# Kernel optimization log

Hardware: AMD Instinct MI355X
Metric: run time of the kernel (lower is better)

Reference implementation:

```python
import jax, jax.numpy as jnp
import numpy as np

B, N, G = 16, 4096, 1024
D1, D2 = 128, 256          # feature1 / feature2 channels
C_IN = D1 + D2             # 384
C_H, C_OUT = 256, 256
BN_EPS = 1e-5


def setup_inputs() -> dict:
    key = jax.random.key(0)
    ks = jax.random.split(key, 10)
    inp = {
        "feature1": jax.random.normal(ks[0], (B, D1, N), jnp.float32),
        "coord1": jax.random.normal(ks[1], (B, 3, N), jnp.float32),
        "feature2": jax.random.normal(ks[2], (B, D2, G), jnp.float32),
        "coord2": jax.random.normal(ks[3], (B, 3, G), jnp.float32),
        # conv1x1 + BN params, layer 1: 384 -> 256
        "W1": jax.random.normal(ks[4], (C_H, C_IN), jnp.float32) / np.sqrt(C_IN),
        "b1": jnp.zeros((C_H,), jnp.float32),
        "gamma1": jnp.ones((C_H,), jnp.float32),
        "beta1": jnp.zeros((C_H,), jnp.float32),
        # layer 2: 256 -> 256
        "W2": jax.random.normal(ks[5], (C_OUT, C_H), jnp.float32) / np.sqrt(C_H),
        "b2": jnp.zeros((C_OUT,), jnp.float32),
        "gamma2": jnp.ones((C_OUT,), jnp.float32),
        "beta2": jnp.zeros((C_OUT,), jnp.float32),
    }
    return inp


def _conv_bn_relu(x, W, b, gamma, beta):
    # x: [B, C_in, N]; 1x1 conv == channel GEMM
    y = jnp.einsum('oi,bin->bon', W, x) + b[None, :, None]
    m = y.mean(axis=(0, 2), keepdims=True)           # BN1d train-mode batch stats
    v = y.var(axis=(0, 2), keepdims=True)
    y = (y - m) * jax.lax.rsqrt(v + BN_EPS) * gamma[None, :, None] + beta[None, :, None]
    return jax.nn.relu(y)


def reference(feature1, coord1, feature2, coord2,
              W1, b1, gamma1, beta1, W2, b2, gamma2, beta2):
    c1 = jnp.transpose(coord1, (0, 2, 1))    # [B, N, 3]
    c2 = jnp.transpose(coord2, (0, 2, 1))    # [B, G, 3]
    f2 = jnp.transpose(feature2, (0, 2, 1))  # [B, G, D2]

    # squared pairwise distances [B, N, G]
    d = (jnp.sum(c1 * c1, -1)[:, :, None]
         + jnp.sum(c2 * c2, -1)[:, None, :]
         - 2.0 * jnp.einsum('bnd,bgd->bng', c1, c2))

    # 3 nearest neighbors (smallest distances)
    neg_d, idx = jax.lax.top_k(-d, 3)        # [B, N, 3]
    dists = -neg_d
    recip = 1.0 / (dists + 1e-8)
    weight = recip / jnp.sum(recip, axis=-1, keepdims=True)  # [B, N, 3]

    # gather neighbor features: [B, N, 3, D2]
    gathered = jnp.take_along_axis(f2[:, None, :, :], idx[:, :, :, None], axis=2)
    interp = jnp.sum(gathered * weight[..., None], axis=2)   # [B, N, D2]

    feat = jnp.concatenate([jnp.transpose(feature1, (0, 2, 1)), interp], axis=-1)
    x = jnp.transpose(feat, (0, 2, 1))       # [B, 384, N]

    x = _conv_bn_relu(x, W1, b1, gamma1, beta1)
    x = _conv_bn_relu(x, W2, b2, gamma2, beta2)
    return x
```

## Files before the change

kernel.cpp:

```cpp
#include <hip/hip_runtime.h>

#define DEVI __device__ __forceinline__

typedef unsigned short u16;
typedef unsigned int   u32;
typedef u16  u16x8 __attribute__((ext_vector_type(8)));
typedef u16  u16x4 __attribute__((ext_vector_type(4)));
typedef short bf16x8 __attribute__((ext_vector_type(8)));
typedef float f32x4 __attribute__((ext_vector_type(4)));

static constexpr int BB = 16, NN = 4096, GG = 1024;
static constexpr int D1 = 128, D2 = 256, CIN = 384, CH = 256;

DEVI float bf2f(u16 h) { u32 u = ((u32)h) << 16; float f; __builtin_memcpy(&f, &u, 4); return f; }
DEVI u16 f2bf(float f) {
    u32 u; __builtin_memcpy(&u, &f, 4);
    u32 r = (u + 0x7fffu + ((u >> 16) & 1u)) >> 16;
    return (u16)r;
}

DEVI void gload16(const void* g, void* l) {
    __builtin_amdgcn_global_load_lds((const __attribute__((address_space(1))) void*)g,
                                     (__attribute__((address_space(3))) void*)l, 16, 0, 0);
}

__global__ void k_convw(const float* __restrict__ W1, const float* __restrict__ W2,
                        u16* __restrict__ W1b, u16* __restrict__ W2b) {
    int i = blockIdx.x * 256 + threadIdx.x;
    if (i < CH * CIN) W1b[i] = f2bf(W1[i]);
    int j = i - CH * CIN;
    if (j >= 0 && j < CH * CH) W2b[j] = f2bf(W2[j]);
}

__global__ void k_f2t(const float* __restrict__ f2, u16* __restrict__ f2t) {
    int b = blockIdx.z, ct = blockIdx.y, gt = blockIdx.x;
    __shared__ u16 tile[64][65];
    int t = threadIdx.x; int g = t & 63; int q = t >> 6;
    for (int p = 0; p < 16; ++p) {
        int cl = p * 4 + q;
        tile[g][cl] = f2bf(f2[((size_t)(b * D2 + ct * 64 + cl)) * GG + gt * 64 + g]);
    }
    __syncthreads();
    for (int p = 0; p < 16; ++p) {
        int gl = p * 4 + q;
        f2t[((size_t)(b * GG + gt * 64 + gl)) * D2 + ct * 64 + g] = tile[gl][g];
    }
}

__global__ __launch_bounds__(256) void k_knn(const float* __restrict__ c1, const float* __restrict__ c2,
                                             int* __restrict__ idxo, float* __restrict__ wo) {
    int b = blockIdx.y; int t = threadIdx.x;
    int q = t >> 2, s = t & 3;
    int n = blockIdx.x * 64 + q;
    __shared__ float4 sp[GG];
    __shared__ int mi[256][4];
    const float* cb = c2 + (size_t)b * 3 * GG;
    for (int i = t; i < GG; i += 256) {
        float x = cb[i], y = cb[GG + i], z = cb[2 * GG + i];
        sp[i] = make_float4(x, y, z, x * x + y * y + z * z);
    }
    __syncthreads();
    const float* pb = c1 + (size_t)b * 3 * NN;
    float px = pb[n], py = pb[NN + n], pz = pb[2 * NN + n];
    float pn = px * px + py * py + pz * pz;
    float d0 = 3.4e38f, d1 = 3.4e38f, d2 = 3.4e38f, d3 = 3.4e38f;
    int i0 = 0, i1 = 0, i2 = 0, i3 = 0;
    for (int gb = 0; gb < GG; gb += 16) {
        #pragma unroll
        for (int u = 0; u < 4; ++u) {
            int g = gb + u * 4 + s;
            float4 p = sp[g];
            float dot = px * p.x + py * p.y + pz * p.z;
            float d = pn + p.w - 2.f * dot;
            bool c0 = d < d0, c1 = d < d1, c2 = d < d2, c3 = d < d3;
            d3 = c2 ? d2 : (c3 ? d : d3);  i3 = c2 ? i2 : (c3 ? g : i3);
            d2 = c1 ? d1 : (c2 ? d : d2);  i2 = c1 ? i1 : (c2 ? g : i2);
            d1 = c0 ? d0 : (c1 ? d : d1);  i1 = c0 ? i0 : (c1 ? g : i1);
            d0 = c0 ? d  : d0;             i0 = c0 ? g : i0;
        }
    }
    mi[t][0] = i0; mi[t][1] = i1; mi[t][2] = i2; mi[t][3] = i3;
    __syncthreads();
    if (s == 0) {
        double e0 = 1e300, e1 = 1e300, e2 = 1e300;
        int j0 = 0x7fffffff, j1 = 0x7fffffff, j2 = 0x7fffffff;
        #pragma unroll 4
        for (int k = 0; k < 16; ++k) {
            int g = mi[q * 4 + (k >> 2)][k & 3];
            float4 p = sp[g];
            double dx = (double)px - (double)p.x;
            double dy = (double)py - (double)p.y;
            double dz = (double)pz - (double)p.z;
            double d = dx * dx + dy * dy + dz * dz;
            bool lt2 = d < e2 || (d == e2 && g < j2);
            if (lt2) {
                bool lt1 = d < e1 || (d == e1 && g < j1);
                if (lt1) {
                    e2 = e1; j2 = j1;
                    bool lt0 = d < e0 || (d == e0 && g < j0);
                    if (lt0) { e1 = e0; j1 = j0; e0 = d; j0 = g; }
                    else { e1 = d; j1 = g; }
                } else { e2 = d; j2 = g; }
            }
        }
        float r0 = 1.f / ((float)e0 + 1e-8f);
        float r1 = 1.f / ((float)e1 + 1e-8f);
        float r2 = 1.f / ((float)e2 + 1e-8f);
        float sum = r0 + r1 + r2;
        size_t base = ((size_t)b * NN + n) * 3;
        idxo[base] = j0; idxo[base + 1] = j1; idxo[base + 2] = j2;
        wo[base] = r0 / sum; wo[base + 1] = r1 / sum; wo[base + 2] = r2 / sum;
    }
}

__global__ void k_pack(const float* __restrict__ f1, const u16* __restrict__ f2t,
                       const int* __restrict__ idxo, const float* __restrict__ wo,
                       u16* __restrict__ Xp) {
    int b = blockIdx.y; int n0 = blockIdx.x * 64;
    __shared__ u16 Xt[64][392];
    int t = threadIdx.x; int j = t & 63; int q = t >> 6;
    for (int p = 0; p < 4; ++p) {
        int oct = p * 4 + q; int cb = oct * 8;
        u16x8 o;
        #pragma unroll
        for (int k = 0; k < 8; ++k)
            o[k] = f2bf(f1[((size_t)(b * D1 + cb + k)) * NN + n0 + j]);
        *(u16x8*)&Xt[j][cb] = o;
    }
    size_t bn = (size_t)b * NN + n0 + j;
    int g0 = idxo[bn * 3], g1 = idxo[bn * 3 + 1], g2 = idxo[bn * 3 + 2];
    float w0 = wo[bn * 3], w1 = wo[bn * 3 + 1], w2 = wo[bn * 3 + 2];
    const u16* r0 = f2t + ((size_t)b * GG + g0) * D2;
    const u16* r1 = f2t + ((size_t)b * GG + g1) * D2;
    const u16* r2 = f2t + ((size_t)b * GG + g2) * D2;
    for (int p = 0; p < 8; ++p) {
        int oct = p * 4 + q; int cb = oct * 8;
        u16x8 a = *(const u16x8*)(r0 + cb);
        u16x8 bb = *(const u16x8*)(r1 + cb);
        u16x8 cc = *(const u16x8*)(r2 + cb);
        u16x8 o;
        #pragma unroll
        for (int k = 0; k < 8; ++k)
            o[k] = f2bf(w0 * bf2f(a[k]) + w1 * bf2f(bb[k]) + w2 * bf2f(cc[k]));
        *(u16x8*)&Xt[j][D1 + cb] = o;
    }
    __syncthreads();
    u16* dst = Xp + ((size_t)b * NN + n0) * CIN;
    for (int p = 0; p < 12; ++p) {
        int ci = p * 256 + t;
        int row = ci / 48, ch = ci % 48;
        *(u16x8*)(dst + (size_t)ci * 8) = *(const u16x8*)&Xt[row][ch * 8];
    }
}

template<int K>
__global__ __launch_bounds__(256) void k_gemm(const u16* __restrict__ A, const u16* __restrict__ Bm,
                                              const float* __restrict__ bias, u16* __restrict__ Yp,
                                              float* __restrict__ S1, float* __restrict__ S2) {
    constexpr int NK = K / 32;
    int nt = blockIdx.x, mt = blockIdx.y, b = blockIdx.z;
    int c0 = mt * 128; size_t n0 = (size_t)b * NN + nt * 128;
    __shared__ u16 Al[2][128 * 32], Bl[2][128 * 32];
    __shared__ float sred[4][64], qred[4][64];
    int t = threadIdx.x, lane = t & 63, w = t >> 6;
    int wr = w >> 1, wc = w & 1;
    f32x4 acc[4][4];
    #pragma unroll
    for (int m = 0; m < 4; ++m)
        #pragma unroll
        for (int n = 0; n < 4; ++n) acc[m][n] = (f32x4){0.f, 0.f, 0.f, 0.f};
    int lr = w * 32 + (lane >> 2);
    int lc = (lane & 3) * 8;

    #pragma unroll
    for (int i = 0; i < 2; ++i) {
        gload16(A + (size_t)(c0 + lr + i * 16) * K + lc, &Al[0][(w * 32 + i * 16) * 32]);
        gload16(Bm + (n0 + lr + i * 16) * K + lc, &Bl[0][(w * 32 + i * 16) * 32]);
    }
    __syncthreads();

    for (int ks = 0; ks < NK; ++ks) {
        int cur = ks & 1;
        if (ks + 1 < NK) {
            #pragma unroll
            for (int i = 0; i < 2; ++i) {
                gload16(A + (size_t)(c0 + lr + i * 16) * K + (ks + 1) * 32 + lc, &Al[cur ^ 1][(w * 32 + i * 16) * 32]);
                gload16(Bm + (n0 + lr + i * 16) * K + (ks + 1) * 32 + lc, &Bl[cur ^ 1][(w * 32 + i * 16) * 32]);
            }
        }
        bf16x8 af[4], bfr[4];
        #pragma unroll
        for (int m = 0; m < 4; ++m)
            af[m] = *(const bf16x8*)&Al[cur][(wr * 64 + m * 16 + (lane & 15)) * 32 + (lane >> 4) * 8];
        #pragma unroll
        for (int n = 0; n < 4; ++n)
            bfr[n] = *(const bf16x8*)&Bl[cur][(wc * 64 + n * 16 + (lane & 15)) * 32 + (lane >> 4) * 8];
        #pragma unroll
        for (int m = 0; m < 4; ++m)
            #pragma unroll
            for (int n = 0; n < 4; ++n)
                acc[m][n] = __builtin_amdgcn_mfma_f32_16x16x32_bf16(af[m], bfr[n], acc[m][n], 0, 0, 0);
        __syncthreads();
    }
    float sacc[4][4], qacc[4][4];
    #pragma unroll
    for (int m = 0; m < 4; ++m) {
        int c = c0 + wr * 64 + m * 16 + (lane >> 4) * 4;
        float b0 = bias[c], b1 = bias[c + 1], b2 = bias[c + 2], b3 = bias[c + 3];
        #pragma unroll
        for (int j = 0; j < 4; ++j) { sacc[m][j] = 0.f; qacc[m][j] = 0.f; }
        #pragma unroll
        for (int n = 0; n < 4; ++n) {
            size_t nn = n0 + wc * 64 + n * 16 + (lane & 15);
            f32x4 v = acc[m][n];
            float y0 = v[0] + b0, y1 = v[1] + b1, y2 = v[2] + b2, y3 = v[3] + b3;
            u16x4 o;
            o[0] = f2bf(y0); o[1] = f2bf(y1); o[2] = f2bf(y2); o[3] = f2bf(y3);
            *(u16x4*)(Yp + nn * CH + c) = o;
            sacc[m][0] += y0; qacc[m][0] += y0 * y0;
            sacc[m][1] += y1; qacc[m][1] += y1 * y1;
            sacc[m][2] += y2; qacc[m][2] += y2 * y2;
            sacc[m][3] += y3; qacc[m][3] += y3 * y3;
        }
    }
    #pragma unroll
    for (int m = 0; m < 4; ++m)
        #pragma unroll
        for (int j = 0; j < 4; ++j) {
            float s = sacc[m][j], qv = qacc[m][j];
            #pragma unroll
            for (int mask = 1; mask <= 8; mask <<= 1) {
                s  += __shfl_xor(s, mask);
                qv += __shfl_xor(qv, mask);
            }
            sacc[m][j] = s; qacc[m][j] = qv;
        }
    int g = lane >> 4;
    if ((lane & 15) == 0) {
        #pragma unroll
        for (int m = 0; m < 4; ++m)
            #pragma unroll
            for (int j = 0; j < 4; ++j) {
                sred[w][m * 16 + g * 4 + j] = sacc[m][j];
                qred[w][m * 16 + g * 4 + j] = qacc[m][j];
            }
    }
    __syncthreads();
    if (t < 128) {
        int half = t >> 6, cl = t & 63;
        float s  = sred[half * 2][cl] + sred[half * 2 + 1][cl];
        float qv = qred[half * 2][cl] + qred[half * 2 + 1][cl];
        atomicAdd(&S1[c0 + half * 64 + cl], s);
        atomicAdd(&S2[c0 + half * 64 + cl], qv);
    }
}

__global__ void k_fin(const float* __restrict__ S1, const float* __restrict__ S2,
                      const float* __restrict__ gamma, const float* __restrict__ beta,
                      float* __restrict__ scale, float* __restrict__ shift) {
    int c = threadIdx.x;
    float inv = 1.f / 65536.f;
    float m = S1[c] * inv;
    float v = S2[c] * inv - m * m;
    float sc = gamma[c] * rsqrtf(v + 1e-5f);
    scale[c] = sc; shift[c] = beta[c] - m * sc;
}

__global__ void k_bnrelu(const u16* __restrict__ Y, const float* __restrict__ scale,
                         const float* __restrict__ shift, u16* __restrict__ X2) {
    __shared__ float sc[256], sh[256];
    int t = threadIdx.x;
    sc[t] = scale[t]; sh[t] = shift[t];
    __syncthreads();
    size_t i = ((size_t)blockIdx.x * 256 + t) * 8;
    int c = (int)(i & 255);
    u16x8 v = *(const u16x8*)(Y + i);
    u16x8 o;
    #pragma unroll
    for (int k = 0; k < 8; ++k) {
        float f = fmaxf(sc[c + k] * bf2f(v[k]) + sh[c + k], 0.f);
        o[k] = f2bf(f);
    }
    *(u16x8*)(X2 + i) = o;
}

__global__ void k_final(const u16* __restrict__ Y2, const float* __restrict__ scale,
                        const float* __restrict__ shift, float* __restrict__ out) {
    int b = blockIdx.y, n0 = blockIdx.x * 64;
    __shared__ u16 tile[64 * 256];
    __shared__ float sc[256], sh[256];
    int t = threadIdx.x;
    sc[t] = scale[t]; sh[t] = shift[t];
    #pragma unroll
    for (int p = 0; p < 8; ++p) {
        int r = p * 8 + (t >> 5); int o = t & 31;
        u16x8 v = *(const u16x8*)(Y2 + ((size_t)(b * NN + n0 + r)) * CH + o * 8);
        int osw = o ^ (r & 7);
        *(u16x8*)&tile[r * 256 + osw * 8] = v;
    }
    __syncthreads();
    for (int p = 0; p < 64; ++p) {
        int c = p * 4 + (t >> 6); int n = t & 63;
        int osw = (c >> 3) ^ (n & 7);
        float f = bf2f(tile[n * 256 + osw * 8 + (c & 7)]);
        out[((size_t)(b * CH + c)) * NN + n0 + n] = fmaxf(sc[c] * f + sh[c], 0.f);
    }
}

extern "C" void kernel_launch(void* const* d_in, const int* in_sizes, int n_in,
                              void* d_out, int out_size, void* d_ws, size_t ws_size,
                              hipStream_t stream) {
    const float* f1  = (const float*)d_in[0];
    const float* c1  = (const float*)d_in[1];
    const float* f2  = (const float*)d_in[2];
    const float* c2  = (const float*)d_in[3];
    const float* W1  = (const float*)d_in[4];
    const float* b1  = (const float*)d_in[5];
    const float* g1  = (const float*)d_in[6];
    const float* be1 = (const float*)d_in[7];
    const float* W2  = (const float*)d_in[8];
    const float* b2  = (const float*)d_in[9];
    const float* g2  = (const float*)d_in[10];
    const float* be2 = (const float*)d_in[11];
    float* out = (float*)d_out;
    char* ws = (char*)d_ws;

    u16* Xp    = (u16*)(ws);
    u16* Y1p   = (u16*)(ws + 50331648);
    u16* X2p   = Xp;
    u16* Y2p   = Y1p;
    u16* W1b   = (u16*)(ws + 83886080);
    u16* W2b   = (u16*)(ws + 84082688);
    u16* F2t   = (u16*)(ws + 84213760);
    int*  idxo = (int*)(ws + 92602368);
    float* wo  = (float*)(ws + 93388800);
    float* stats = (float*)(ws + 94175232);
    float* S1a = stats,        *S2a = stats + 256;
    float* S1b = stats + 512,  *S2b = stats + 768;
    float* sc1 = stats + 1024, *sh1 = stats + 1280;
    float* sc2 = stats + 1536, *sh2 = stats + 1792;

    hipMemsetAsync(stats, 0, 4096, stream);
    k_convw<<<640, 256, 0, stream>>>(W1, W2, W1b, W2b);
    k_f2t<<<dim3(16, 4, 16), 256, 0, stream>>>(f2, F2t);
    k_knn<<<dim3(64, 16), 256, 0, stream>>>(c1, c2, idxo, wo);
    k_pack<<<dim3(64, 16), 256, 0, stream>>>(f1, F2t, idxo, wo, Xp);
    k_gemm<CIN><<<dim3(32, 2, 16), 256, 0, stream>>>(W1b, Xp, b1, Y1p, S1a, S2a);
    k_fin<<<1, 256, 0, stream>>>(S1a, S2a, g1, be1, sc1, sh1);
    k_bnrelu<<<8192, 256, 0, stream>>>(Y1p, sc1, sh1, X2p);
    k_gemm<CH><<<dim3(32, 2, 16), 256, 0, stream>>>(W2b, X2p, b2, Y2p, S1b, S2b);
    k_fin<<<1, 256, 0, stream>>>(S1b, S2b, g2, be2, sc2, sh2);
    k_final<<<dim3(64, 16), 256, 0, stream>>>(Y2p, sc2, sh2, out);
}
```

Baseline: 292.2 us.

## Pack kNN distance+index into u32 keys and stage GEMM output through LDS

The kNN inner loop now packs the truncated, clamped distance bits together with the 10-bit index into one u32 key. It keeps a sorted top-4 with min/max chains instead of paired float/int selects, which cuts VALU work per candidate. The later double-precision refinement over the 16 candidates still fixes the exact order. Separately, the GEMM epilogue writes bf16 results into a reused, XOR-swizzled LDS buffer and then stores full 16-byte rows to global, replacing scattered 8-byte stores. The risk is that truncating the distance bits could drop a true neighbor from the top-4 candidates, and the epilogue adds LDS traffic.

After: 274.0 us. 6.2% less time.

```diff
diff --git a/kernel.cpp b/kernel.cpp
--- a/kernel.cpp
+++ b/kernel.cpp
@@ -53,7 +53,7 @@
     int q = t >> 2, s = t & 3;
     int n = blockIdx.x * 64 + q;
     __shared__ float4 sp[GG];
-    __shared__ int mi[256][4];
+    __shared__ u32 mi[256][4];
     const float* cb = c2 + (size_t)b * 3 * GG;
     for (int i = t; i < GG; i += 256) {
         float x = cb[i], y = cb[GG + i], z = cb[2 * GG + i];
@@ -63,30 +63,30 @@
     const float* pb = c1 + (size_t)b * 3 * NN;
     float px = pb[n], py = pb[NN + n], pz = pb[2 * NN + n];
     float pn = px * px + py * py + pz * pz;
-    float d0 = 3.4e38f, d1 = 3.4e38f, d2 = 3.4e38f, d3 = 3.4e38f;
-    int i0 = 0, i1 = 0, i2 = 0, i3 = 0;
+    u32 k0 = 0xFFFFFFFFu, k1 = 0xFFFFFFFFu, k2 = 0xFFFFFFFFu, k3 = 0xFFFFFFFFu;
     for (int gb = 0; gb < GG; gb += 16) {
         #pragma unroll
         for (int u = 0; u < 4; ++u) {
             int g = gb + u * 4 + s;
             float4 p = sp[g];
             float dot = px * p.x + py * p.y + pz * p.z;
-            float d = pn + p.w - 2.f * dot;
-            bool c0 = d < d0, c1 = d < d1, c2 = d < d2, c3 = d < d3;
-            d3 = c2 ? d2 : (c3 ? d : d3);  i3 = c2 ? i2 : (c3 ? g : i3);
-            d2 = c1 ? d1 : (c2 ? d : d2);  i2 = c1 ? i1 : (c2 ? g : i2);
-            d1 = c0 ? d0 : (c1 ? d : d1);  i1 = c0 ? i0 : (c1 ? g : i1);
-            d0 = c0 ? d  : d0;             i0 = c0 ? g : i0;
-        }
-    }
-    mi[t][0] = i0; mi[t][1] = i1; mi[t][2] = i2; mi[t][3] = i3;
+            float d = fmaxf(pn + p.w - 2.f * dot, 0.f);
+            u32 bits; __builtin_memcpy(&bits, &d, 4);
+            u32 key = (bits & 0xFFFFFC00u) | (u32)g;
+            u32 u0 = max(k0, key); k0 = min(k0, key);
+            u32 u1 = max(k1, u0);  k1 = min(k1, u0);
+            u32 u2 = max(k2, u1);  k2 = min(k2, u1);
+            k3 = min(k3, u2);
+        }
+    }
+    mi[t][0] = k0; mi[t][1] = k1; mi[t][2] = k2; mi[t][3] = k3;
     __syncthreads();
     if (s == 0) {
         double e0 = 1e300, e1 = 1e300, e2 = 1e300;
         int j0 = 0x7fffffff, j1 = 0x7fffffff, j2 = 0x7fffffff;
         #pragma unroll 4
         for (int k = 0; k < 16; ++k) {
-            int g = mi[q * 4 + (k >> 2)][k & 3];
+            int g = (int)(mi[q * 4 + (k >> 2)][k & 3] & 1023u);
             float4 p = sp[g];
             double dx = (double)px - (double)p.x;
             double dy = (double)py - (double)p.y;
@@ -160,7 +160,7 @@
     constexpr int NK = K / 32;
     int nt = blockIdx.x, mt = blockIdx.y, b = blockIdx.z;
     int c0 = mt * 128; size_t n0 = (size_t)b * NN + nt * 128;
-    __shared__ u16 Al[2][128 * 32], Bl[2][128 * 32];
+    __shared__ u16 smem[16384];
     __shared__ float sred[4][64], qred[4][64];
     int t = threadIdx.x, lane = t & 63, w = t >> 6;
     int wr = w >> 1, wc = w & 1;
@@ -174,27 +174,29 @@
 
     #pragma unroll
     for (int i = 0; i < 2; ++i) {
-        gload16(A + (size_t)(c0 + lr + i * 16) * K + lc, &Al[0][(w * 32 + i * 16) * 32]);
-        gload16(Bm + (n0 + lr + i * 16) * K + lc, &Bl[0][(w * 32 + i * 16) * 32]);
+        gload16(A + (size_t)(c0 + lr + i * 16) * K + lc, &smem[(w * 32 + i * 16) * 32]);
+        gload16(Bm + (n0 + lr + i * 16) * K + lc, &smem[8192 + (w * 32 + i * 16) * 32]);
     }
     __syncthreads();
 
     for (int ks = 0; ks < NK; ++ks) {
         int cur = ks & 1;
+        int an = 4096 * (cur ^ 1), bn2 = 8192 + 4096 * (cur ^ 1);
+        int ac = 4096 * cur,       bc  = 8192 + 4096 * cur;
         if (ks + 1 < NK) {
             #pragma unroll
             for (int i = 0; i < 2; ++i) {
-                gload16(A + (size_t)(c0 + lr + i * 16) * K + (ks + 1) * 32 + lc, &Al[cur ^ 1][(w * 32 + i * 16) * 32]);
-                gload16(Bm + (n0 + lr + i * 16) * K + (ks + 1) * 32 + lc, &Bl[cur ^ 1][(w * 32 + i * 16) * 32]);
+                gload16(A + (size_t)(c0 + lr + i * 16) * K + (ks + 1) * 32 + lc, &smem[an + (w * 32 + i * 16) * 32]);
+                gload16(Bm + (n0 + lr + i * 16) * K + (ks + 1) * 32 + lc, &smem[bn2 + (w * 32 + i * 16) * 32]);
             }
         }
         bf16x8 af[4], bfr[4];
         #pragma unroll
         for (int m = 0; m < 4; ++m)
-            af[m] = *(const bf16x8*)&Al[cur][(wr * 64 + m * 16 + (lane & 15)) * 32 + (lane >> 4) * 8];
+            af[m] = *(const bf16x8*)&smem[ac + (wr * 64 + m * 16 + (lane & 15)) * 32 + (lane >> 4) * 8];
         #pragma unroll
         for (int n = 0; n < 4; ++n)
-            bfr[n] = *(const bf16x8*)&Bl[cur][(wc * 64 + n * 16 + (lane & 15)) * 32 + (lane >> 4) * 8];
+            bfr[n] = *(const bf16x8*)&smem[bc + (wc * 64 + n * 16 + (lane & 15)) * 32 + (lane >> 4) * 8];
         #pragma unroll
         for (int m = 0; m < 4; ++m)
             #pragma unroll
@@ -206,17 +208,18 @@
     #pragma unroll
     for (int m = 0; m < 4; ++m) {
         int c = c0 + wr * 64 + m * 16 + (lane >> 4) * 4;
+        int clocal = wr * 64 + m * 16 + (lane >> 4) * 4;
         float b0 = bias[c], b1 = bias[c + 1], b2 = bias[c + 2], b3 = bias[c + 3];
         #pragma unroll
         for (int j = 0; j < 4; ++j) { sacc[m][j] = 0.f; qacc[m][j] = 0.f; }
         #pragma unroll
         for (int n = 0; n < 4; ++n) {
-            size_t nn = n0 + wc * 64 + n * 16 + (lane & 15);
+            int r = wc * 64 + n * 16 + (lane & 15);
             f32x4 v = acc[m][n];
             float y0 = v[0] + b0, y1 = v[1] + b1, y2 = v[2] + b2, y3 = v[3] + b3;
             u16x4 o;
             o[0] = f2bf(y0); o[1] = f2bf(y1); o[2] = f2bf(y2); o[3] = f2bf(y3);
-            *(u16x4*)(Yp + nn * CH + c) = o;
+            *(u16x4*)&smem[r * 128 + (clocal ^ ((r & 7) << 3))] = o;
             sacc[m][0] += y0; qacc[m][0] += y0 * y0;
             sacc[m][1] += y1; qacc[m][1] += y1 * y1;
             sacc[m][2] += y2; qacc[m][2] += y2 * y2;
@@ -246,6 +249,13 @@
             }
     }
     __syncthreads();
+    #pragma unroll
+    for (int p = 0; p < 8; ++p) {
+        int r = p * 16 + (t >> 4);
+        int chunk = t & 15;
+        u16x8 v = *(const u16x8*)&smem[r * 128 + ((chunk * 8) ^ ((r & 7) << 3))];
+        *(u16x8*)(Yp + (n0 + r) * CH + c0 + chunk * 8) = v;
+    }
     if (t < 128) {
         int half = t >> 6, cl = t & 63;
         float s  = sred[half * 2][cl] + sred[half * 2 + 1][cl];
@@ -340,7 +350,7 @@
     float* sc1 = stats + 1024, *sh1 = stats + 1280;
     float* sc2 = stats + 1536, *sh2 = stats + 1792;
 
-    hipMemsetAsync(stats, 0, 4096, stream);
+    (void)hipMemsetAsync(stats, 0, 4096, stream);
     k_convw<<<640, 256, 0, stream>>>(W1, W2, W1b, W2b);
     k_f2t<<<dim3(16, 4, 16), 256, 0, stream>>>(f2, F2t);
     k_knn<<<dim3(64, 16), 256, 0, stream>>>(c1, c2, idxo, wo);
```
